# Optimization experiments

Measured on AMD Instinct MI355X. Metric: run time of the kernel, lower is better.

Reference implementation:

```python
import jax, jax.numpy as jnp
import numpy as np


def setup_inputs() -> dict:
    key = jax.random.key(0)
    k1, k2, k3 = jax.random.split(key, 3)
    B, S, D = 128, 1024, 64
    return {
        "q": jax.random.normal(k1, (B, S, D), dtype=jnp.float32),
        "k": jax.random.normal(k2, (B, S, D), dtype=jnp.float32),
        "v": jax.random.normal(k3, (B, S, D), dtype=jnp.float32),
    }


def reference(q, k, v):
    # Faithful to the torch module: NO 1/sqrt(d) scaling.
    # Chunking over batch dim in the original is math-equivalent to full bmm.
    scores = jnp.einsum("bsd,btd->bst", q, k)  # [B, S, S]
    attn = jax.nn.softmax(scores, axis=-1)
    return jnp.einsum("bst,btd->bsd", attn, v)  # [B, S, D]
```

## Files before the change

### kernel.cpp

```cpp
#include <hip/hip_runtime.h>
#include <math.h>

namespace {

typedef _Float16 half8 __attribute__((ext_vector_type(8)));
typedef float floatx4 __attribute__((ext_vector_type(4)));

constexpr int kS   = 1024;
constexpr int kD   = 64;
constexpr int kPad = 72;
constexpr float kLog2e = 1.4426950408889634f;
constexpr float kThr   = 8.0f;

union H4 { _Float16 h[4]; uint2 u2; };

__device__ __forceinline__ float fast_exp2(float x) {
#if __has_builtin(__builtin_amdgcn_exp2f)
  return __builtin_amdgcn_exp2f(x);
#else
  return exp2f(x);
#endif
}

__device__ __forceinline__ float fast_rcp(float x) {
#if __has_builtin(__builtin_amdgcn_rcpf)
  return __builtin_amdgcn_rcpf(x);
#else
  return 1.0f / x;
#endif
}

__global__ __launch_bounds__(256, 2)
void fa_mfma_kernel(const float* __restrict__ qg, const float* __restrict__ kg,
                    const float* __restrict__ vg, float* __restrict__ og) {
  __shared__ __align__(16) _Float16 sK [64][kPad];
  __shared__ __align__(16) _Float16 sVt[64][kPad];
  __shared__ __align__(16) _Float16 sP [256][kPad];

  const int tid  = threadIdx.x;
  const int lane = tid & 63;
  const int w    = __builtin_amdgcn_readfirstlane(tid >> 6);
  const int quad = lane >> 4;
  const int r    = lane & 15;

  const int blk = blockIdx.x;
  const int b     = (blk & 7) + 8 * (blk >> 5);
  const int qbase = ((blk >> 3) & 3) * 256;

  const float* qb = qg + (size_t)b * kS * kD;
  const float* kb = kg + (size_t)b * kS * kD;
  const float* vb = vg + (size_t)b * kS * kD;
  float*       ob = og + (size_t)b * kS * kD;

  half8 fqh[4][2], fql[4][2];
#pragma unroll
  for (int ntq = 0; ntq < 4; ++ntq)
#pragma unroll
    for (int ks = 0; ks < 2; ++ks) {
      const float* src =
          qb + (size_t)(qbase + w * 64 + ntq * 16 + r) * kD + ks * 32 + quad * 8;
      float4 a = ((const float4*)src)[0];
      float4 c = ((const float4*)src)[1];
      float f[8] = {a.x, a.y, a.z, a.w, c.x, c.y, c.z, c.w};
#pragma unroll
      for (int j = 0; j < 8; ++j) {
        float x = f[j] * kLog2e;
        _Float16 h = (_Float16)x;
        fqh[ntq][ks][j] = h;
        fql[ntq][ks][j] = (_Float16)(x - (float)h);
      }
    }

  float m_i[4] = {-INFINITY, -INFINITY, -INFINITY, -INFINITY};
  float l_i[4] = {0.f, 0.f, 0.f, 0.f};
  floatx4 O[4][4];
#pragma unroll
  for (int a = 0; a < 4; ++a)
#pragma unroll
    for (int c = 0; c < 4; ++c) O[a][c] = floatx4{0.f, 0.f, 0.f, 0.f};

  const int krow = tid >> 2, kc0 = (tid & 3) * 16;
  const int vkey4 = (tid & 15) * 4;
  const int vd0   = (tid >> 4) * 4;
  float4 kbuf[4], vbuf[4];
  {
    const float4* ksrc = (const float4*)(kb + (size_t)krow * kD + kc0);
#pragma unroll
    for (int g = 0; g < 4; ++g) kbuf[g] = ksrc[g];
#pragma unroll
    for (int kk = 0; kk < 4; ++kk)
      vbuf[kk] = *(const float4*)(vb + (size_t)(vkey4 + kk) * kD + vd0);
  }

  for (int kt = 0; kt < kS / 64; ++kt) {
    __syncthreads();
#pragma unroll
    for (int g = 0; g < 4; ++g) {
      float t[4] = {kbuf[g].x, kbuf[g].y, kbuf[g].z, kbuf[g].w};
      H4 hk;
#pragma unroll
      for (int j = 0; j < 4; ++j) hk.h[j] = (_Float16)t[j];
      *(uint2*)&sK[krow][kc0 + g * 4] = hk.u2;
    }
    {
      float tv[4][4];
#pragma unroll
      for (int kk = 0; kk < 4; ++kk) {
        tv[kk][0] = vbuf[kk].x; tv[kk][1] = vbuf[kk].y;
        tv[kk][2] = vbuf[kk].z; tv[kk][3] = vbuf[kk].w;
      }
#pragma unroll
      for (int j = 0; j < 4; ++j) {
        H4 hv;
#pragma unroll
        for (int kk = 0; kk < 4; ++kk) hv.h[kk] = (_Float16)tv[kk][j];
        *(uint2*)&sVt[vd0 + j][vkey4] = hv.u2;
      }
    }
    {
      const int ktn = (kt + 1) & 15;
      const float4* ksrc =
          (const float4*)(kb + (size_t)(ktn * 64 + krow) * kD + kc0);
#pragma unroll
      for (int g = 0; g < 4; ++g) kbuf[g] = ksrc[g];
#pragma unroll
      for (int kk = 0; kk < 4; ++kk)
        vbuf[kk] =
            *(const float4*)(vb + (size_t)(ktn * 64 + vkey4 + kk) * kD + vd0);
    }
    __syncthreads();

#pragma unroll
    for (int h = 0; h < 2; ++h) {
      floatx4 S[2][4];
      __builtin_amdgcn_s_setprio(1);
#pragma unroll
      for (int mt = 0; mt < 4; ++mt) {
        half8 fk0 = *(const half8*)&sK[mt * 16 + r][0 * 32 + quad * 8];
        half8 fk1 = *(const half8*)&sK[mt * 16 + r][1 * 32 + quad * 8];
#pragma unroll
        for (int g = 0; g < 2; ++g) {
          const int ntq = h * 2 + g;
          floatx4 ah = {0.f, 0.f, 0.f, 0.f}, al = {0.f, 0.f, 0.f, 0.f};
          ah = __builtin_amdgcn_mfma_f32_16x16x32_f16(fk0, fqh[ntq][0], ah, 0, 0, 0);
          ah = __builtin_amdgcn_mfma_f32_16x16x32_f16(fk1, fqh[ntq][1], ah, 0, 0, 0);
          al = __builtin_amdgcn_mfma_f32_16x16x32_f16(fk0, fql[ntq][0], al, 0, 0, 0);
          al = __builtin_amdgcn_mfma_f32_16x16x32_f16(fk1, fql[ntq][1], al, 0, 0, 0);
          S[g][mt] = ah + al;
        }
      }
      __builtin_amdgcn_s_setprio(0);

      float tm[2];
#pragma unroll
      for (int g = 0; g < 2; ++g) {
        float t = -INFINITY;
#pragma unroll
        for (int mt = 0; mt < 4; ++mt)
#pragma unroll
          for (int j = 0; j < 4; ++j) t = fmaxf(t, S[g][mt][j]);
        t = fmaxf(t, __shfl_xor(t, 16, 64));
        t = fmaxf(t, __shfl_xor(t, 32, 64));
        tm[g] = t;
      }
      const unsigned long long need =
          __ballot(tm[0] > m_i[h * 2] + kThr || tm[1] > m_i[h * 2 + 1] + kThr);
      if (need) {
        float alpha[2];
#pragma unroll
        for (int g = 0; g < 2; ++g) {
          const int ntq = h * 2 + g;
          const float mn = fmaxf(m_i[ntq], tm[g]);
          alpha[g] = fast_exp2(m_i[ntq] - mn);
          m_i[ntq] = mn;
          l_i[ntq] *= alpha[g];
        }
#pragma unroll
        for (int g = 0; g < 2; ++g) {
          const int mtq = h * 2 + g;
#pragma unroll
          for (int j = 0; j < 4; ++j) {
            const float a = __shfl(alpha[g], quad * 4 + j, 64);
#pragma unroll
            for (int nd = 0; nd < 4; ++nd) O[mtq][nd][j] *= a;
          }
        }
      }
#pragma unroll
      for (int g = 0; g < 2; ++g) {
        const int ntq = h * 2 + g;
        float rs = 0.f;
#pragma unroll
        for (int mt = 0; mt < 4; ++mt) {
          H4 hp;
#pragma unroll
          for (int j = 0; j < 4; ++j) {
            float pj = fast_exp2(S[g][mt][j] - m_i[ntq]);
            rs += pj;
            hp.h[j] = (_Float16)pj;
          }
          *(uint2*)&sP[w * 64 + ntq * 16 + r][mt * 16 + quad * 4] = hp.u2;
        }
        rs += __shfl_xor(rs, 16, 64);
        rs += __shfl_xor(rs, 32, 64);
        l_i[ntq] += rs;
      }
    }

    __builtin_amdgcn_s_setprio(1);
#pragma unroll
    for (int ks = 0; ks < 2; ++ks) {
      half8 fp[4];
#pragma unroll
      for (int mtq = 0; mtq < 4; ++mtq)
        fp[mtq] = *(const half8*)&sP[w * 64 + mtq * 16 + r][ks * 32 + quad * 8];
#pragma unroll
      for (int nd = 0; nd < 4; ++nd) {
        half8 fv = *(const half8*)&sVt[nd * 16 + r][ks * 32 + quad * 8];
#pragma unroll
        for (int mtq = 0; mtq < 4; ++mtq)
          O[mtq][nd] =
              __builtin_amdgcn_mfma_f32_16x16x32_f16(fp[mtq], fv, O[mtq][nd], 0, 0, 0);
      }
    }
    __builtin_amdgcn_s_setprio(0);
  }

#pragma unroll
  for (int mtq = 0; mtq < 4; ++mtq)
#pragma unroll
    for (int j = 0; j < 4; ++j) {
      const float lrow = __shfl(l_i[mtq], quad * 4 + j, 64);
      const float linv = fast_rcp(lrow);
      float* dst =
          ob + (size_t)(qbase + w * 64 + mtq * 16 + quad * 4 + j) * kD + r;
#pragma unroll
      for (int nd = 0; nd < 4; ++nd) dst[nd * 16] = O[mtq][nd][j] * linv;
    }
}

}

extern "C" void kernel_launch(void* const* d_in, const int* in_sizes, int n_in,
                              void* d_out, int out_size, void* d_ws, size_t ws_size,
                              hipStream_t stream) {
  const float* q = (const float*)d_in[0];
  const float* k = (const float*)d_in[1];
  const float* v = (const float*)d_in[2];
  float* out = (float*)d_out;

  fa_mfma_kernel<<<dim3(512), 256, 0, stream>>>(q, k, v, out);
}
```

Baseline: 172.7 us.

## Double-buffer K/V in LDS and interleave QK and PV across row halves

Doubles the shared-memory K and V^T tiles so the next tile is staged while the current one is consumed, which removes one barrier per iteration. The loop is restructured so that the QK MFMAs for the second half of query rows are issued before the PV MFMAs for the first half, letting softmax work overlap with matrix work. The V fragments are loaded once and reused for both halves. This raises LDS use and register pressure (S0, S1, fv are live together), which may hurt occupancy at 2 blocks per CU.

```diff
diff --git a/kernel.cpp b/kernel.cpp
--- a/kernel.cpp
+++ b/kernel.cpp
@@ -33,8 +33,8 @@
 __global__ __launch_bounds__(256, 2)
 void fa_mfma_kernel(const float* __restrict__ qg, const float* __restrict__ kg,
                     const float* __restrict__ vg, float* __restrict__ og) {
-  __shared__ __align__(16) _Float16 sK [64][kPad];
-  __shared__ __align__(16) _Float16 sVt[64][kPad];
+  __shared__ __align__(16) _Float16 sK [2][64][kPad];
+  __shared__ __align__(16) _Float16 sVt[2][64][kPad];
   __shared__ __align__(16) _Float16 sP [256][kPad];
 
   const int tid  = threadIdx.x;
@@ -83,74 +83,68 @@
   const int vkey4 = (tid & 15) * 4;
   const int vd0   = (tid >> 4) * 4;
   float4 kbuf[4], vbuf[4];
-  {
-    const float4* ksrc = (const float4*)(kb + (size_t)krow * kD + kc0);
+
+  auto load_kv = [&](int kt) {
+    const float4* ksrc = (const float4*)(kb + (size_t)(kt * 64 + krow) * kD + kc0);
 #pragma unroll
     for (int g = 0; g < 4; ++g) kbuf[g] = ksrc[g];
 #pragma unroll
     for (int kk = 0; kk < 4; ++kk)
-      vbuf[kk] = *(const float4*)(vb + (size_t)(vkey4 + kk) * kD + vd0);
-  }
-
-  for (int kt = 0; kt < kS / 64; ++kt) {
-    __syncthreads();
+      vbuf[kk] = *(const float4*)(vb + (size_t)(kt * 64 + vkey4 + kk) * kD + vd0);
+  };
+  auto stage = [&](int bi) {
 #pragma unroll
     for (int g = 0; g < 4; ++g) {
       float t[4] = {kbuf[g].x, kbuf[g].y, kbuf[g].z, kbuf[g].w};
       H4 hk;
 #pragma unroll
       for (int j = 0; j < 4; ++j) hk.h[j] = (_Float16)t[j];
-      *(uint2*)&sK[krow][kc0 + g * 4] = hk.u2;
-    }
+      *(uint2*)&sK[bi][krow][kc0 + g * 4] = hk.u2;
+    }
+    float tv[4][4];
+#pragma unroll
+    for (int kk = 0; kk < 4; ++kk) {
+      tv[kk][0] = vbuf[kk].x; tv[kk][1] = vbuf[kk].y;
+      tv[kk][2] = vbuf[kk].z; tv[kk][3] = vbuf[kk].w;
+    }
+#pragma unroll
+    for (int j = 0; j < 4; ++j) {
+      H4 hv;
+#pragma unroll
+      for (int kk = 0; kk < 4; ++kk) hv.h[kk] = (_Float16)tv[kk][j];
+      *(uint2*)&sVt[bi][vd0 + j][vkey4] = hv.u2;
+    }
+  };
+
+  load_kv(0);
+  stage(0);
+  load_kv(1);
+
+  for (int kt = 0; kt < kS / 64; ++kt) {
+    const int cur = kt & 1, nxt = cur ^ 1;
+    __syncthreads();
+    stage(nxt);
+    load_kv((kt + 2) & 15);
+
+    floatx4 S0[2][4];
+    __builtin_amdgcn_s_setprio(1);
+#pragma unroll
+    for (int mt = 0; mt < 4; ++mt) {
+      half8 fk0 = *(const half8*)&sK[cur][mt * 16 + r][quad * 8];
+      half8 fk1 = *(const half8*)&sK[cur][mt * 16 + r][32 + quad * 8];
+#pragma unroll
+      for (int g = 0; g < 2; ++g) {
+        floatx4 ah = {0.f, 0.f, 0.f, 0.f}, al = {0.f, 0.f, 0.f, 0.f};
+        ah = __builtin_amdgcn_mfma_f32_16x16x32_f16(fk0, fqh[g][0], ah, 0, 0, 0);
+        ah = __builtin_amdgcn_mfma_f32_16x16x32_f16(fk1, fqh[g][1], ah, 0, 0, 0);
+        al = __builtin_amdgcn_mfma_f32_16x16x32_f16(fk0, fql[g][0], al, 0, 0, 0);
+        al = __builtin_amdgcn_mfma_f32_16x16x32_f16(fk1, fql[g][1], al, 0, 0, 0);
+        S0[g][mt] = ah + al;
+      }
+    }
+    __builtin_amdgcn_s_setprio(0);
+
     {
-      float tv[4][4];
-#pragma unroll
-      for (int kk = 0; kk < 4; ++kk) {
-        tv[kk][0] = vbuf[kk].x; tv[kk][1] = vbuf[kk].y;
-        tv[kk][2] = vbuf[kk].z; tv[kk][3] = vbuf[kk].w;
-      }
-#pragma unroll
-      for (int j = 0; j < 4; ++j) {
-        H4 hv;
-#pragma unroll
-        for (int kk = 0; kk < 4; ++kk) hv.h[kk] = (_Float16)tv[kk][j];
-        *(uint2*)&sVt[vd0 + j][vkey4] = hv.u2;
-      }
-    }
-    {
-      const int ktn = (kt + 1) & 15;
-      const float4* ksrc =
-          (const float4*)(kb + (size_t)(ktn * 64 + krow) * kD + kc0);
-#pragma unroll
-      for (int g = 0; g < 4; ++g) kbuf[g] = ksrc[g];
-#pragma unroll
-      for (int kk = 0; kk < 4; ++kk)
-        vbuf[kk] =
-            *(const float4*)(vb + (size_t)(ktn * 64 + vkey4 + kk) * kD + vd0);
-    }
-    __syncthreads();
-
-#pragma unroll
-    for (int h = 0; h < 2; ++h) {
-      floatx4 S[2][4];
-      __builtin_amdgcn_s_setprio(1);
-#pragma unroll
-      for (int mt = 0; mt < 4; ++mt) {
-        half8 fk0 = *(const half8*)&sK[mt * 16 + r][0 * 32 + quad * 8];
-        half8 fk1 = *(const half8*)&sK[mt * 16 + r][1 * 32 + quad * 8];
-#pragma unroll
-        for (int g = 0; g < 2; ++g) {
-          const int ntq = h * 2 + g;
-          floatx4 ah = {0.f, 0.f, 0.f, 0.f}, al = {0.f, 0.f, 0.f, 0.f};
-          ah = __builtin_amdgcn_mfma_f32_16x16x32_f16(fk0, fqh[ntq][0], ah, 0, 0, 0);
-          ah = __builtin_amdgcn_mfma_f32_16x16x32_f16(fk1, fqh[ntq][1], ah, 0, 0, 0);
-          al = __builtin_amdgcn_mfma_f32_16x16x32_f16(fk0, fql[ntq][0], al, 0, 0, 0);
-          al = __builtin_amdgcn_mfma_f32_16x16x32_f16(fk1, fql[ntq][1], al, 0, 0, 0);
-          S[g][mt] = ah + al;
-        }
-      }
-      __builtin_amdgcn_s_setprio(0);
-
       float tm[2];
 #pragma unroll
       for (int g = 0; g < 2; ++g) {
@@ -158,69 +152,146 @@
 #pragma unroll
         for (int mt = 0; mt < 4; ++mt)
 #pragma unroll
-          for (int j = 0; j < 4; ++j) t = fmaxf(t, S[g][mt][j]);
+          for (int j = 0; j < 4; ++j) t = fmaxf(t, S0[g][mt][j]);
         t = fmaxf(t, __shfl_xor(t, 16, 64));
         t = fmaxf(t, __shfl_xor(t, 32, 64));
         tm[g] = t;
       }
       const unsigned long long need =
-          __ballot(tm[0] > m_i[h * 2] + kThr || tm[1] > m_i[h * 2 + 1] + kThr);
+          __ballot(tm[0] > m_i[0] + kThr || tm[1] > m_i[1] + kThr);
       if (need) {
         float alpha[2];
 #pragma unroll
         for (int g = 0; g < 2; ++g) {
-          const int ntq = h * 2 + g;
-          const float mn = fmaxf(m_i[ntq], tm[g]);
-          alpha[g] = fast_exp2(m_i[ntq] - mn);
-          m_i[ntq] = mn;
-          l_i[ntq] *= alpha[g];
+          const float mn = fmaxf(m_i[g], tm[g]);
+          alpha[g] = fast_exp2(m_i[g] - mn);
+          m_i[g] = mn;
+          l_i[g] *= alpha[g];
         }
 #pragma unroll
-        for (int g = 0; g < 2; ++g) {
-          const int mtq = h * 2 + g;
+        for (int g = 0; g < 2; ++g)
 #pragma unroll
           for (int j = 0; j < 4; ++j) {
             const float a = __shfl(alpha[g], quad * 4 + j, 64);
 #pragma unroll
-            for (int nd = 0; nd < 4; ++nd) O[mtq][nd][j] *= a;
+            for (int nd = 0; nd < 4; ++nd) O[g][nd][j] *= a;
           }
-        }
-      }
-#pragma unroll
-      for (int g = 0; g < 2; ++g) {
-        const int ntq = h * 2 + g;
+      }
+#pragma unroll
+      for (int g = 0; g < 2; ++g) {
         float rs = 0.f;
 #pragma unroll
         for (int mt = 0; mt < 4; ++mt) {
           H4 hp;
 #pragma unroll
           for (int j = 0; j < 4; ++j) {
-            float pj = fast_exp2(S[g][mt][j] - m_i[ntq]);
+            float pj = fast_exp2(S0[g][mt][j] - m_i[g]);
             rs += pj;
             hp.h[j] = (_Float16)pj;
           }
-          *(uint2*)&sP[w * 64 + ntq * 16 + r][mt * 16 + quad * 4] = hp.u2;
+          *(uint2*)&sP[w * 64 + g * 16 + r][mt * 16 + quad * 4] = hp.u2;
         }
         rs += __shfl_xor(rs, 16, 64);
         rs += __shfl_xor(rs, 32, 64);
-        l_i[ntq] += rs;
-      }
-    }
-
+        l_i[g] += rs;
+      }
+    }
+
+    floatx4 S1[2][4];
     __builtin_amdgcn_s_setprio(1);
 #pragma unroll
+    for (int mt = 0; mt < 4; ++mt) {
+      half8 fk0 = *(const half8*)&sK[cur][mt * 16 + r][quad * 8];
+      half8 fk1 = *(const half8*)&sK[cur][mt * 16 + r][32 + quad * 8];
+#pragma unroll
+      for (int g = 0; g < 2; ++g) {
+        floatx4 ah = {0.f, 0.f, 0.f, 0.f}, al = {0.f, 0.f, 0.f, 0.f};
+        ah = __builtin_amdgcn_mfma_f32_16x16x32_f16(fk0, fqh[2 + g][0], ah, 0, 0, 0);
+        ah = __builtin_amdgcn_mfma_f32_16x16x32_f16(fk1, fqh[2 + g][1], ah, 0, 0, 0);
+        al = __builtin_amdgcn_mfma_f32_16x16x32_f16(fk0, fql[2 + g][0], al, 0, 0, 0);
+        al = __builtin_amdgcn_mfma_f32_16x16x32_f16(fk1, fql[2 + g][1], al, 0, 0, 0);
+        S1[g][mt] = ah + al;
+      }
+    }
+    __builtin_amdgcn_s_setprio(0);
+
+    half8 fv[2][4];
+    __builtin_amdgcn_s_setprio(1);
+#pragma unroll
     for (int ks = 0; ks < 2; ++ks) {
-      half8 fp[4];
-#pragma unroll
-      for (int mtq = 0; mtq < 4; ++mtq)
-        fp[mtq] = *(const half8*)&sP[w * 64 + mtq * 16 + r][ks * 32 + quad * 8];
+      half8 fp0 = *(const half8*)&sP[w * 64 + 0 * 16 + r][ks * 32 + quad * 8];
+      half8 fp1 = *(const half8*)&sP[w * 64 + 1 * 16 + r][ks * 32 + quad * 8];
 #pragma unroll
       for (int nd = 0; nd < 4; ++nd) {
-        half8 fv = *(const half8*)&sVt[nd * 16 + r][ks * 32 + quad * 8];
-#pragma unroll
-        for (int mtq = 0; mtq < 4; ++mtq)
-          O[mtq][nd] =
-              __builtin_amdgcn_mfma_f32_16x16x32_f16(fp[mtq], fv, O[mtq][nd], 0, 0, 0);
+        fv[ks][nd] = *(const half8*)&sVt[cur][nd * 16 + r][ks * 32 + quad * 8];
+        O[0][nd] = __builtin_amdgcn_mfma_f32_16x16x32_f16(fp0, fv[ks][nd], O[0][nd], 0, 0, 0);
+        O[1][nd] = __builtin_amdgcn_mfma_f32_16x16x32_f16(fp1, fv[ks][nd], O[1][nd], 0, 0, 0);
+      }
+    }
+    __builtin_amdgcn_s_setprio(0);
+
+    {
+      float tm[2];
+#pragma unroll
+      for (int g = 0; g < 2; ++g) {
+        float t = -INFINITY;
+#pragma unroll
+        for (int mt = 0; mt < 4; ++mt)
+#pragma unroll
+          for (int j = 0; j < 4; ++j) t = fmaxf(t, S1[g][mt][j]);
+        t = fmaxf(t, __shfl_xor(t, 16, 64));
+        t = fmaxf(t, __shfl_xor(t, 32, 64));
+        tm[g] = t;
+      }
+      const unsigned long long need =
+          __ballot(tm[0] > m_i[2] + kThr || tm[1] > m_i[3] + kThr);
+      if (need) {
+        float alpha[2];
+#pragma unroll
+        for (int g = 0; g < 2; ++g) {
+          const float mn = fmaxf(m_i[2 + g], tm[g]);
+          alpha[g] = fast_exp2(m_i[2 + g] - mn);
+          m_i[2 + g] = mn;
+          l_i[2 + g] *= alpha[g];
+        }
+#pragma unroll
+        for (int g = 0; g < 2; ++g)
+#pragma unroll
+          for (int j = 0; j < 4; ++j) {
+            const float a = __shfl(alpha[g], quad * 4 + j, 64);
+#pragma unroll
+            for (int nd = 0; nd < 4; ++nd) O[2 + g][nd][j] *= a;
+          }
+      }
+#pragma unroll
+      for (int g = 0; g < 2; ++g) {
+        float rs = 0.f;
+#pragma unroll
+        for (int mt = 0; mt < 4; ++mt) {
+          H4 hp;
+#pragma unroll
+          for (int j = 0; j < 4; ++j) {
+            float pj = fast_exp2(S1[g][mt][j] - m_i[2 + g]);
+            rs += pj;
+            hp.h[j] = (_Float16)pj;
+          }
+          *(uint2*)&sP[w * 64 + (2 + g) * 16 + r][mt * 16 + quad * 4] = hp.u2;
+        }
+        rs += __shfl_xor(rs, 16, 64);
+        rs += __shfl_xor(rs, 32, 64);
+        l_i[2 + g] += rs;
+      }
+    }
+
+    __builtin_amdgcn_s_setprio(1);
+#pragma unroll
+    for (int ks = 0; ks < 2; ++ks) {
+      half8 fp2 = *(const half8*)&sP[w * 64 + 2 * 16 + r][ks * 32 + quad * 8];
+      half8 fp3 = *(const half8*)&sP[w * 64 + 3 * 16 + r][ks * 32 + quad * 8];
+#pragma unroll
+      for (int nd = 0; nd < 4; ++nd) {
+        O[2][nd] = __builtin_amdgcn_mfma_f32_16x16x32_f16(fp2, fv[ks][nd], O[2][nd], 0, 0, 0);
+        O[3][nd] = __builtin_amdgcn_mfma_f32_16x16x32_f16(fp3, fv[ks][nd], O[3][nd], 0, 0, 0);
       }
     }
     __builtin_amdgcn_s_setprio(0);
```

After: 197.4 us. 1.14x slower.
